# Kernel tuning notes

Hardware: AMD Instinct MI355X
Metric: run time of the kernel (lower is better)

The kernel has to match this reference:

```python
import jax, jax.numpy as jnp
import numpy as np

NUM_HEADS = 12
HEAD_DIM = 64
HIDDEN = 768
SLOT_DIM = 30
BS = 8
FULL = SLOT_DIM * BS  # 240
SLOT_LEN = 32
LEN0 = 512   # slot-broadcast cache length
LEN1 = 128   # per-sample cache length


def tf_slot(x, slot_dim):
    # (slot_dim*bs, H, L, h) -> (bs, H, slot_dim*L, h)
    full, nh, L, h = x.shape
    bs = full // slot_dim
    x = x.reshape(slot_dim, bs, nh, L, h).transpose(1, 2, 0, 3, 4)
    return x.reshape(bs, nh, slot_dim * L, h)


def back_slot(x, slot_dim):
    # (bs, H, slot_dim*L, h) -> (slot_dim*bs, H, L, h)
    bs, nh, total, h = x.shape
    L = total // slot_dim
    x = x.reshape(bs, nh, slot_dim, L, h).transpose(2, 0, 1, 3, 4)
    return x.reshape(slot_dim * bs, nh, L, h)


def setup_inputs() -> dict:
    key = jax.random.key(0)
    ks = jax.random.split(key, 12)
    s = 0.02
    return {
        "hidden_states": jax.random.normal(ks[0], (FULL, SLOT_LEN, HIDDEN), jnp.float32),
        "attention_mask": jnp.zeros((FULL, 1, 1, LEN0 + LEN1 + SLOT_LEN), jnp.float32),
        "cache0_key": jax.random.normal(ks[1], (BS, NUM_HEADS, LEN0, HEAD_DIM), jnp.float32),
        "cache0_value": jax.random.normal(ks[2], (BS, NUM_HEADS, LEN0, HEAD_DIM), jnp.float32),
        "cache1_key": jax.random.normal(ks[3], (FULL, NUM_HEADS, LEN1, HEAD_DIM), jnp.float32),
        "cache1_value": jax.random.normal(ks[4], (FULL, NUM_HEADS, LEN1, HEAD_DIM), jnp.float32),
        "Wq": jax.random.normal(ks[5], (HIDDEN, HIDDEN), jnp.float32) * s,
        "bq": jax.random.normal(ks[6], (HIDDEN,), jnp.float32) * s,
        "Wk": jax.random.normal(ks[7], (HIDDEN, HIDDEN), jnp.float32) * s,
        "bk": jax.random.normal(ks[8], (HIDDEN,), jnp.float32) * s,
        "Wv": jax.random.normal(ks[9], (HIDDEN, HIDDEN), jnp.float32) * s,
        "bv": jax.random.normal(ks[10], (HIDDEN,), jnp.float32) * s,
        "slot_dim": SLOT_DIM,
    }


def reference(hidden_states, attention_mask, cache0_key, cache0_value,
              cache1_key, cache1_value, Wq, bq, Wk, bk, Wv, bv, slot_dim):
    B, L, hid = hidden_states.shape

    def split_heads(x):  # (B, L, hid) -> (B, H, L, h)
        return x.reshape(B, L, NUM_HEADS, HEAD_DIM).transpose(0, 2, 1, 3)

    q = split_heads(hidden_states @ Wq + bq)
    k = split_heads(hidden_states @ Wk + bk)
    v = split_heads(hidden_states @ Wv + bv)

    # self-attention scores (B, H, L, L)
    self_scores = jnp.einsum('bhqd,bhkd->bhqk', q, k)

    # cache0: slot-broadcast path (cache batch = bs, queries batch = slot_dim*bs)
    q_tf = tf_slot(q, slot_dim)  # (bs, H, slot_dim*L, h)
    s0 = back_slot(jnp.einsum('bhqd,bhkd->bhqk', q_tf, cache0_key), slot_dim)  # (B,H,L,LEN0)
    # cache1: direct path (matching batch)
    s1 = jnp.einsum('bhqd,bhkd->bhqk', q, cache1_key)  # (B,H,L,LEN1)

    scores = jnp.concatenate([s0, s1, self_scores], axis=-1)
    scores = scores / jnp.sqrt(jnp.float32(HEAD_DIM)) + attention_mask
    probs = jax.nn.softmax(scores, axis=-1)  # single softmax over all KV sources

    len0 = cache0_key.shape[2]
    len1 = cache1_key.shape[2]
    # self context
    ctx = jnp.einsum('bhqk,bhkd->bhqd', probs[..., -L:], v)
    # cache0 context via slot transform
    p0 = tf_slot(probs[..., :len0], slot_dim)  # (bs, H, slot_dim*L, LEN0)
    ctx = ctx + back_slot(jnp.einsum('bhqk,bhkd->bhqd', p0, cache0_value), slot_dim)
    # cache1 context direct
    ctx = ctx + jnp.einsum('bhqk,bhkd->bhqd', probs[..., len0:len0 + len1], cache1_value)

    # (B, H, L, h) -> (B, L, hid)
    return ctx.transpose(0, 2, 1, 3).reshape(B, L, hid)
```

## Files before the change

### kernel.cpp

```cpp
#include <hip/hip_runtime.h>
#include <math.h>

#define NUM_HEADS 12
#define HEAD_DIM  64
#define HIDDEN    768
#define BS        8
#define FULL      240
#define SLOT_LEN  32
#define LEN0      512
#define LEN1      128
#define KTOT      672
#define M_TOK     (FULL * SLOT_LEN)

typedef float f32x4 __attribute__((ext_vector_type(4)));
typedef short s16x8 __attribute__((ext_vector_type(8)));
typedef short s16x4 __attribute__((ext_vector_type(4)));

__device__ __forceinline__ short f2bf(float x) {
    unsigned u = __float_as_uint(x);
    unsigned r = (u + 0x7fffu + ((u >> 16) & 1u)) >> 16;
    return (short)r;
}

__device__ __forceinline__ void gll16(const short* g, short* l) {
    __builtin_amdgcn_global_load_lds(
        (const __attribute__((address_space(1))) unsigned int*)g,
        (__attribute__((address_space(3))) unsigned int*)l, 16, 0, 0);
}

__global__ __launch_bounds__(256) void cast_hs(const float* __restrict__ in,
                                               short* __restrict__ out, int n4) {
    int i = blockIdx.x * 256 + threadIdx.x;
    if (i < n4) {
        float4 v = ((const float4*)in)[i];
        s16x4 o = {f2bf(v.x), f2bf(v.y), f2bf(v.z), f2bf(v.w)};
        ((s16x4*)out)[i] = o;
    }
}

__global__ __launch_bounds__(256) void trans_v0(const float* __restrict__ v0,
                                                short* __restrict__ v0t) {
    __shared__ float tile[32][65];
    const size_t base = (size_t)blockIdx.x * 2048;
    const int t = threadIdx.x;
#pragma unroll
    for (int i = 0; i < 2; ++i) {
        int f = t + i * 256;
        int kr = f >> 4, d4 = (f & 15) * 4;
        float4 v = *(const float4*)&v0[base + kr * 64 + d4];
        tile[kr][d4 + 0] = v.x; tile[kr][d4 + 1] = v.y;
        tile[kr][d4 + 2] = v.z; tile[kr][d4 + 3] = v.w;
    }
    __syncthreads();
#pragma unroll
    for (int i = 0; i < 2; ++i) {
        int g = t + i * 256;
        int d = g >> 3, kr4 = (g & 7) * 4;
        s16x4 o = {f2bf(tile[kr4 + 0][d]), f2bf(tile[kr4 + 1][d]),
                   f2bf(tile[kr4 + 2][d]), f2bf(tile[kr4 + 3][d])};
        *(s16x4*)&v0t[base + d * 32 + kr4] = o;
    }
}

__global__ __launch_bounds__(256) void cast_w_t(const float* __restrict__ Wq,
                                                const float* __restrict__ Wk,
                                                const float* __restrict__ Wv,
                                                short* __restrict__ WtAll) {
    const float* W = (blockIdx.z == 0) ? Wq : (blockIdx.z == 1) ? Wk : Wv;
    short* Wt = WtAll + (size_t)blockIdx.z * HIDDEN * HIDDEN;
    __shared__ __align__(16) float tile[32][33];
    const int kb0 = blockIdx.y * 32, nb0 = blockIdx.x * 32;
    const int r = threadIdx.x >> 3, c4 = (threadIdx.x & 7) * 4;
    float4 v = *(const float4*)&W[(size_t)(kb0 + r) * HIDDEN + nb0 + c4];
    tile[r][c4 + 0] = v.x; tile[r][c4 + 1] = v.y;
    tile[r][c4 + 2] = v.z; tile[r][c4 + 3] = v.w;
    __syncthreads();
    s16x4 o = {f2bf(tile[c4 + 0][r]), f2bf(tile[c4 + 1][r]),
               f2bf(tile[c4 + 2][r]), f2bf(tile[c4 + 3][r])};
    *(s16x4*)&Wt[(size_t)(nb0 + r) * HIDDEN + kb0 + c4] = o;
}

__global__ __launch_bounds__(256) void qkv_mfma(
    const short* __restrict__ hsb, const short* __restrict__ WtAll,
    const float* __restrict__ bq, const float* __restrict__ bk,
    const float* __restrict__ bv,
    short* __restrict__ qo, short* __restrict__ ko, short* __restrict__ vo)
{
    const int z = blockIdx.z;
    const short* Wt = WtAll + (size_t)z * HIDDEN * HIDDEN;
    const float* bias = (z == 0) ? bq : (z == 1) ? bk : bv;
    short* outp = (z == 0) ? qo : (z == 1) ? ko : vo;

    __shared__ __align__(16) short smem[128 * 128];
    short* As = smem;
    short* Bs = smem + 128 * 64;

    const int t = threadIdx.x;
    const int lane = t & 63, w = t >> 6;
    const int l15 = lane & 15, quad = lane >> 4;
    const int mBase = blockIdx.y * 128, nBase = blockIdx.x * 128;
    const int mw = (w & 1) * 64, nw = (w >> 1) * 64;

    const int srow_in = lane >> 3;
    const int scol8 = (lane & 7) ^ srow_in;

    f32x4 acc[4][4];
    const f32x4 z4 = {0.f, 0.f, 0.f, 0.f};
#pragma unroll
    for (int i = 0; i < 4; ++i)
#pragma unroll
        for (int j = 0; j < 4; ++j) acc[i][j] = z4;

    for (int kb = 0; kb < HIDDEN; kb += 64) {
        __syncthreads();
#pragma unroll
        for (int j = 0; j < 4; ++j) {
            int row = w * 32 + j * 8 + srow_in;
            gll16(&hsb[(size_t)(mBase + row) * HIDDEN + kb + scol8 * 8],
                  &As[(w * 32 + j * 8) * 64]);
            gll16(&Wt[(size_t)(nBase + row) * HIDDEN + kb + scol8 * 8],
                  &Bs[(w * 32 + j * 8) * 64]);
        }
        __syncthreads();
#pragma unroll
        for (int kc = 0; kc < 2; ++kc) {
            s16x8 a[4], b[4];
#pragma unroll
            for (int mt = 0; mt < 4; ++mt) {
                int row = mw + mt * 16 + l15;
                int c8 = (kc * 4 + quad) ^ (row & 7);
                a[mt] = *(const s16x8*)&As[row * 64 + c8 * 8];
            }
#pragma unroll
            for (int nt = 0; nt < 4; ++nt) {
                int row = nw + nt * 16 + l15;
                int c8 = (kc * 4 + quad) ^ (row & 7);
                b[nt] = *(const s16x8*)&Bs[row * 64 + c8 * 8];
            }
#pragma unroll
            for (int mt = 0; mt < 4; ++mt)
#pragma unroll
                for (int nt = 0; nt < 4; ++nt)
                    acc[mt][nt] = __builtin_amdgcn_mfma_f32_16x16x32_bf16(
                        a[mt], b[nt], acc[mt][nt], 0, 0, 0);
        }
    }

    __syncthreads();
#pragma unroll
    for (int nt = 0; nt < 4; ++nt) {
        float bvv = bias[nBase + nw + nt * 16 + l15];
        int col = nw + nt * 16 + l15;
#pragma unroll
        for (int mt = 0; mt < 4; ++mt)
#pragma unroll
            for (int r = 0; r < 4; ++r) {
                int row = mw + mt * 16 + quad * 4 + r;
                smem[row * 128 + col] = f2bf(acc[mt][nt][r] + bvv);
            }
    }
    __syncthreads();
#pragma unroll
    for (int i = 0; i < 8; ++i) {
        int f = t + i * 256;
        int row = f >> 4, c8 = (f & 15) * 8;
        uint4 val = *(const uint4*)&smem[row * 128 + c8];
        int m = mBase + row, n = nBase + c8;
        size_t dst = (((size_t)(m >> 5) * NUM_HEADS + (n >> 6)) * SLOT_LEN + (m & 31)) * 64 + (n & 63);
        *(uint4*)&outp[dst] = val;
    }
}

__global__ __launch_bounds__(256) void attn_mfma(
    const short* __restrict__ qb, const short* __restrict__ kbuf,
    const short* __restrict__ vbuf,
    const short* __restrict__ k0c, const short* __restrict__ v0t,
    const float* __restrict__ c1k, const float* __restrict__ c1v,
    const float* __restrict__ mask, float* __restrict__ out)
{
    __shared__ __align__(16) short Klds[4][32][72];
    __shared__ __align__(16) short Vt[4][64][40];
    __shared__ __align__(16) short Plds[4][32][36];

    const int t = threadIdx.x, lane = t & 63, w = t >> 6;
    const int task = blockIdx.x * 4 + w;
    const int B = task / 12, h = task % 12;
    const int l15 = lane & 15, quad = lane >> 4;

    const short* qp  = qb  + (size_t)(B * NUM_HEADS + h) * SLOT_LEN * 64;
    const short* ksp = kbuf + (size_t)(B * NUM_HEADS + h) * SLOT_LEN * 64;
    const short* vsp = vbuf + (size_t)(B * NUM_HEADS + h) * SLOT_LEN * 64;
    const short* k0p = k0c + (size_t)((B & 7) * NUM_HEADS + h) * LEN0 * 64;
    const short* v0p = v0t + (size_t)((B & 7) * NUM_HEADS + h) * LEN0 * 64;
    const float* k1p = c1k + (size_t)(B * NUM_HEADS + h) * LEN1 * 64;
    const float* v1p = c1v + (size_t)(B * NUM_HEADS + h) * LEN1 * 64;
    const float* mp  = mask + (size_t)B * KTOT;

    short (*K)[72] = Klds[w];
    short (*V)[40] = Vt[w];
    short (*P)[36] = Plds[w];

    const int skey = lane >> 4;
    const int sc4 = (lane & 15) << 2;

    const int kkey = lane >> 3, ku = lane & 7;
    const int vd = lane >> 2, vu = lane & 3;

    s16x8 qf[2][2];
#pragma unroll
    for (int qh = 0; qh < 2; ++qh)
#pragma unroll
        for (int kc = 0; kc < 2; ++kc)
            qf[qh][kc] = *(const s16x8*)&qp[(qh * 16 + l15) * 64 + kc * 32 + quad * 8];

    const f32x4 z4 = {0.f, 0.f, 0.f, 0.f};
    f32x4 o[2][4];
    float lpart[2][4];
#pragma unroll
    for (int qh = 0; qh < 2; ++qh) {
#pragma unroll
        for (int dq = 0; dq < 4; ++dq) o[qh][dq] = z4;
#pragma unroll
        for (int r = 0; r < 4; ++r) lpart[qh][r] = 0.f;
    }

    s16x8 kpre[4], vpre[4];
    float4 kreg[8];
    float mreg0, mreg1;

    auto issue_bf = [&](int c) {
        const short* kcb = k0p + c * 2048;
        const short* vcb = v0p + c * 2048;
#pragma unroll
        for (int i = 0; i < 4; ++i) {
            kpre[i] = *(const s16x8*)&kcb[(i * 64 + lane) * 8];
            vpre[i] = *(const s16x8*)&vcb[(i * 64 + lane) * 8];
        }
    };
    auto issue_k1 = [&](int c) {
        const float* sk = k1p + (c - 16) * 2048;
#pragma unroll
        for (int i = 0; i < 8; ++i)
            kreg[i] = *(const float4*)&sk[(i * 4 + skey) * 64 + sc4];
    };
    auto issue_mask = [&](int c) {
        mreg0 = mp[c * 32 + l15];
        mreg1 = mp[c * 32 + 16 + l15];
    };

    issue_bf(0);
    issue_mask(0);

    for (int c = 0; c < 21; ++c) {
        const float mv0 = mreg0, mv1 = mreg1;
        float4 vv[8];
        bool f32path = (c >= 16 && c < 20);

        if (c < 16) {
#pragma unroll
            for (int i = 0; i < 4; ++i)
                *(s16x8*)&K[i * 8 + kkey][ku * 8] = kpre[i];
#pragma unroll
            for (int i = 0; i < 4; ++i)
                *(s16x8*)&V[i * 16 + vd][vu * 8] = vpre[i];
        } else if (c < 20) {
#pragma unroll
            for (int i = 0; i < 8; ++i) {
                s16x4 kk = {f2bf(kreg[i].x), f2bf(kreg[i].y), f2bf(kreg[i].z), f2bf(kreg[i].w)};
                *(s16x4*)&K[i * 4 + skey][sc4] = kk;
            }
            const float* sv = v1p + (c - 16) * 2048;
#pragma unroll
            for (int i = 0; i < 8; ++i)
                vv[i] = *(const float4*)&sv[(i * 4 + skey) * 64 + sc4];
        } else {
#pragma unroll
            for (int i = 0; i < 8; ++i) {
                int key = i * 4 + skey;
                *(s16x4*)&K[key][sc4] = *(const s16x4*)&ksp[key * 64 + sc4];
            }
            short vtmp[32];
#pragma unroll
            for (int key = 0; key < 32; ++key) vtmp[key] = vsp[key * 64 + lane];
#pragma unroll
            for (int k4 = 0; k4 < 8; ++k4) {
                s16x4 vo4 = {vtmp[k4 * 4 + 0], vtmp[k4 * 4 + 1],
                             vtmp[k4 * 4 + 2], vtmp[k4 * 4 + 3]};
                *(s16x4*)&V[lane][k4 * 4] = vo4;
            }
        }

        if (c + 1 < 16)      issue_bf(c + 1);
        else if (c + 1 < 20) issue_k1(c + 1);
        if (c + 1 < 21)      issue_mask(c + 1);

        f32x4 s[2][2];
#pragma unroll
        for (int qh = 0; qh < 2; ++qh)
#pragma unroll
            for (int kh = 0; kh < 2; ++kh) s[qh][kh] = z4;
#pragma unroll
        for (int kh = 0; kh < 2; ++kh) {
            s16x8 kf0 = *(const s16x8*)&K[kh * 16 + l15][quad * 8];
            s16x8 kf1 = *(const s16x8*)&K[kh * 16 + l15][32 + quad * 8];
#pragma unroll
            for (int qh = 0; qh < 2; ++qh) {
                s[qh][kh] = __builtin_amdgcn_mfma_f32_16x16x32_bf16(qf[qh][0], kf0, s[qh][kh], 0, 0, 0);
                s[qh][kh] = __builtin_amdgcn_mfma_f32_16x16x32_bf16(qf[qh][1], kf1, s[qh][kh], 0, 0, 0);
            }
        }

#pragma unroll
        for (int qh = 0; qh < 2; ++qh)
#pragma unroll
            for (int kh = 0; kh < 2; ++kh) {
                float mv = kh ? mv1 : mv0;
#pragma unroll
                for (int r = 0; r < 4; ++r) {
                    float p = __expf(s[qh][kh][r] * 0.125f + mv);
                    lpart[qh][r] += p;
                    P[qh * 16 + quad * 4 + r][kh * 16 + l15] = f2bf(p);
                }
            }

        if (f32path) {
#pragma unroll
            for (int i = 0; i < 8; ++i) {
                int key = i * 4 + skey;
                V[sc4 + 0][key] = f2bf(vv[i].x);
                V[sc4 + 1][key] = f2bf(vv[i].y);
                V[sc4 + 2][key] = f2bf(vv[i].z);
                V[sc4 + 3][key] = f2bf(vv[i].w);
            }
        }

#pragma unroll
        for (int qh = 0; qh < 2; ++qh) {
            s16x4 plo = *(const s16x4*)&P[qh * 16 + l15][quad * 8];
            s16x4 phi = *(const s16x4*)&P[qh * 16 + l15][quad * 8 + 4];
            s16x8 pf = __builtin_shufflevector(plo, phi, 0, 1, 2, 3, 4, 5, 6, 7);
#pragma unroll
            for (int dq = 0; dq < 4; ++dq) {
                s16x8 vf = *(const s16x8*)&V[dq * 16 + l15][quad * 8];
                o[qh][dq] = __builtin_amdgcn_mfma_f32_16x16x32_bf16(pf, vf, o[qh][dq], 0, 0, 0);
            }
        }
    }

    float linv[2][4];
#pragma unroll
    for (int qh = 0; qh < 2; ++qh)
#pragma unroll
        for (int r = 0; r < 4; ++r) {
            float l = lpart[qh][r];
            l += __shfl_xor(l, 1);
            l += __shfl_xor(l, 2);
            l += __shfl_xor(l, 4);
            l += __shfl_xor(l, 8);
            linv[qh][r] = 1.f / l;
        }

#pragma unroll
    for (int qh = 0; qh < 2; ++qh)
#pragma unroll
        for (int dq = 0; dq < 4; ++dq)
#pragma unroll
            for (int r = 0; r < 4; ++r) {
                int row = qh * 16 + quad * 4 + r;
                out[((size_t)B * SLOT_LEN + row) * HIDDEN + h * 64 + dq * 16 + l15] =
                    o[qh][dq][r] * linv[qh][r];
            }
}

extern "C" void kernel_launch(void* const* d_in, const int* in_sizes, int n_in,
                              void* d_out, int out_size, void* d_ws, size_t ws_size,
                              hipStream_t stream) {
    const float* hs   = (const float*)d_in[0];
    const float* mask = (const float*)d_in[1];
    const float* c0k  = (const float*)d_in[2];
    const float* c0v  = (const float*)d_in[3];
    const float* c1k  = (const float*)d_in[4];
    const float* c1v  = (const float*)d_in[5];
    const float* Wq   = (const float*)d_in[6];
    const float* bq   = (const float*)d_in[7];
    const float* Wk   = (const float*)d_in[8];
    const float* bk   = (const float*)d_in[9];
    const float* Wv   = (const float*)d_in[10];
    const float* bv   = (const float*)d_in[11];
    float* out = (float*)d_out;

    short* hsb = (short*)d_ws;
    short* WtA = hsb + (size_t)M_TOK * HIDDEN;
    short* qb  = WtA + (size_t)3 * HIDDEN * HIDDEN;
    short* kbw = qb + (size_t)M_TOK * HIDDEN;
    short* vbw = kbw + (size_t)M_TOK * HIDDEN;
    short* k0c = (short*)d_ws;
    short* v0t = k0c + (size_t)BS * NUM_HEADS * LEN0 * HEAD_DIM;

    cast_hs<<<(M_TOK * HIDDEN / 4 + 255) / 256, 256, 0, stream>>>(hs, hsb, M_TOK * HIDDEN / 4);
    cast_w_t<<<dim3(24, 24, 3), 256, 0, stream>>>(Wq, Wk, Wv, WtA);
    qkv_mfma<<<dim3(HIDDEN / 128, M_TOK / 128, 3), 256, 0, stream>>>(
        hsb, WtA, bq, bk, bv, qb, kbw, vbw);
    {
        int n4 = BS * NUM_HEADS * LEN0 * HEAD_DIM / 4;
        cast_hs<<<(n4 + 255) / 256, 256, 0, stream>>>(c0k, k0c, n4);
        trans_v0<<<BS * NUM_HEADS * (LEN0 / 32), 256, 0, stream>>>(c0v, v0t);
    }
    attn_mfma<<<720, 256, 0, stream>>>(qb, kbw, vbw, k0c, v0t, c1k, c1v, mask, out);
}
```

Baseline: 362.1 us.

## XOR-swizzle LDS tiles for K, V, P and pre-swizzle cache0 layouts

Replaces the padded LDS arrays for K, V and P with unpadded tiles that use XOR swizzling, which avoids bank conflicts while using less shared memory. The cache0 key cast and value transpose kernels now write their output in the swizzled order, so the attention kernel can copy chunks straight into LDS. Softmax switches to exp2 with the log2e factor folded into the scale and the mask. The next-chunk prefetch issue is also moved into each branch. The risk is that the swizzle index maths must match exactly across the producer kernels and every LDS read and write.

```diff
diff --git a/kernel.cpp b/kernel.cpp
--- a/kernel.cpp
+++ b/kernel.cpp
@@ -38,6 +38,19 @@
     }
 }
 
+__global__ __launch_bounds__(256) void cast_k0(const float* __restrict__ k0,
+                                               short* __restrict__ k0c) {
+    const size_t base = (size_t)blockIdx.x * 2048;
+    const int t = threadIdx.x;
+    const int row = t >> 3, c8 = t & 7;
+    const float* src = &k0[base + row * 64 + c8 * 8];
+    float4 a = *(const float4*)src;
+    float4 b = *(const float4*)(src + 4);
+    s16x8 o = {f2bf(a.x), f2bf(a.y), f2bf(a.z), f2bf(a.w),
+               f2bf(b.x), f2bf(b.y), f2bf(b.z), f2bf(b.w)};
+    *(s16x8*)&k0c[base + row * 64 + (size_t)((c8 ^ (row & 7)) * 8)] = o;
+}
+
 __global__ __launch_bounds__(256) void trans_v0(const float* __restrict__ v0,
                                                 short* __restrict__ v0t) {
     __shared__ float tile[32][65];
@@ -58,7 +71,8 @@
         int d = g >> 3, kr4 = (g & 7) * 4;
         s16x4 o = {f2bf(tile[kr4 + 0][d]), f2bf(tile[kr4 + 1][d]),
                    f2bf(tile[kr4 + 2][d]), f2bf(tile[kr4 + 3][d])};
-        *(s16x4*)&v0t[base + d * 32 + kr4] = o;
+        int grp = (kr4 >> 3) ^ ((d >> 1) & 3);
+        *(s16x4*)&v0t[base + d * 32 + grp * 8 + (kr4 & 7)] = o;
     }
 }
 
@@ -178,9 +192,9 @@
     const float* __restrict__ c1k, const float* __restrict__ c1v,
     const float* __restrict__ mask, float* __restrict__ out)
 {
-    __shared__ __align__(16) short Klds[4][32][72];
-    __shared__ __align__(16) short Vt[4][64][40];
-    __shared__ __align__(16) short Plds[4][32][36];
+    __shared__ __align__(16) short Klds[4][32][64];
+    __shared__ __align__(16) short Vt[4][64][32];
+    __shared__ __align__(16) short Plds[4][32][32];
 
     const int t = threadIdx.x, lane = t & 63, w = t >> 6;
     const int task = blockIdx.x * 4 + w;
@@ -196,15 +210,14 @@
     const float* v1p = c1v + (size_t)(B * NUM_HEADS + h) * LEN1 * 64;
     const float* mp  = mask + (size_t)B * KTOT;
 
-    short (*K)[72] = Klds[w];
-    short (*V)[40] = Vt[w];
-    short (*P)[36] = Plds[w];
+    short (*K)[64] = Klds[w];
+    short (*V)[32] = Vt[w];
+    short (*P)[32] = Plds[w];
+    short* Kf = &K[0][0];
+    short* Vf = &V[0][0];
 
     const int skey = lane >> 4;
     const int sc4 = (lane & 15) << 2;
-
-    const int kkey = lane >> 3, ku = lane & 7;
-    const int vd = lane >> 2, vu = lane & 3;
 
     s16x8 qf[2][2];
 #pragma unroll
@@ -227,6 +240,9 @@
     s16x8 kpre[4], vpre[4];
     float4 kreg[8];
     float mreg0, mreg1;
+
+    const float LOG2E = 1.4426950408889634f;
+    const float SCL   = 0.125f * 1.4426950408889634f;
 
     auto issue_bf = [&](int c) {
         const short* kcb = k0p + c * 2048;
@@ -244,8 +260,8 @@
             kreg[i] = *(const float4*)&sk[(i * 4 + skey) * 64 + sc4];
     };
     auto issue_mask = [&](int c) {
-        mreg0 = mp[c * 32 + l15];
-        mreg1 = mp[c * 32 + 16 + l15];
+        mreg0 = mp[c * 32 + l15] * LOG2E;
+        mreg1 = mp[c * 32 + 16 + l15] * LOG2E;
     };
 
     issue_bf(0);
@@ -259,25 +275,30 @@
         if (c < 16) {
 #pragma unroll
             for (int i = 0; i < 4; ++i)
-                *(s16x8*)&K[i * 8 + kkey][ku * 8] = kpre[i];
+                *(s16x8*)&Kf[(i * 64 + lane) * 8] = kpre[i];
 #pragma unroll
             for (int i = 0; i < 4; ++i)
-                *(s16x8*)&V[i * 16 + vd][vu * 8] = vpre[i];
+                *(s16x8*)&Vf[(i * 64 + lane) * 8] = vpre[i];
+            if (c + 1 < 16) issue_bf(c + 1);
+            if (c == 15) issue_k1(16);
         } else if (c < 20) {
 #pragma unroll
             for (int i = 0; i < 8; ++i) {
                 s16x4 kk = {f2bf(kreg[i].x), f2bf(kreg[i].y), f2bf(kreg[i].z), f2bf(kreg[i].w)};
-                *(s16x4*)&K[i * 4 + skey][sc4] = kk;
+                int row = i * 4 + skey;
+                *(s16x4*)&K[row][((l15 >> 1) ^ (row & 7)) * 8 + (l15 & 1) * 4] = kk;
             }
             const float* sv = v1p + (c - 16) * 2048;
 #pragma unroll
             for (int i = 0; i < 8; ++i)
                 vv[i] = *(const float4*)&sv[(i * 4 + skey) * 64 + sc4];
+            if (c + 1 < 20) issue_k1(c + 1);
         } else {
 #pragma unroll
             for (int i = 0; i < 8; ++i) {
                 int key = i * 4 + skey;
-                *(s16x4*)&K[key][sc4] = *(const s16x4*)&ksp[key * 64 + sc4];
+                *(s16x4*)&K[key][((l15 >> 1) ^ (key & 7)) * 8 + (l15 & 1) * 4] =
+                    *(const s16x4*)&ksp[key * 64 + sc4];
             }
             short vtmp[32];
 #pragma unroll
@@ -286,13 +307,12 @@
             for (int k4 = 0; k4 < 8; ++k4) {
                 s16x4 vo4 = {vtmp[k4 * 4 + 0], vtmp[k4 * 4 + 1],
                              vtmp[k4 * 4 + 2], vtmp[k4 * 4 + 3]};
-                *(s16x4*)&V[lane][k4 * 4] = vo4;
-            }
-        }
-
-        if (c + 1 < 16)      issue_bf(c + 1);
-        else if (c + 1 < 20) issue_k1(c + 1);
-        if (c + 1 < 21)      issue_mask(c + 1);
+                int grp = (k4 >> 1) ^ ((lane >> 1) & 3);
+                *(s16x4*)&V[lane][grp * 8 + (k4 & 1) * 4] = vo4;
+            }
+        }
+
+        if (c + 1 < 21) issue_mask(c + 1);
 
         f32x4 s[2][2];
 #pragma unroll
@@ -301,8 +321,9 @@
             for (int kh = 0; kh < 2; ++kh) s[qh][kh] = z4;
 #pragma unroll
         for (int kh = 0; kh < 2; ++kh) {
-            s16x8 kf0 = *(const s16x8*)&K[kh * 16 + l15][quad * 8];
-            s16x8 kf1 = *(const s16x8*)&K[kh * 16 + l15][32 + quad * 8];
+            int rowk = kh * 16 + l15;
+            s16x8 kf0 = *(const s16x8*)&K[rowk][(quad ^ (rowk & 7)) * 8];
+            s16x8 kf1 = *(const s16x8*)&K[rowk][((4 + quad) ^ (rowk & 7)) * 8];
 #pragma unroll
             for (int qh = 0; qh < 2; ++qh) {
                 s[qh][kh] = __builtin_amdgcn_mfma_f32_16x16x32_bf16(qf[qh][0], kf0, s[qh][kh], 0, 0, 0);
@@ -317,9 +338,11 @@
                 float mv = kh ? mv1 : mv0;
 #pragma unroll
                 for (int r = 0; r < 4; ++r) {
-                    float p = __expf(s[qh][kh][r] * 0.125f + mv);
+                    float p = exp2f(fmaf(s[qh][kh][r], SCL, mv));
                     lpart[qh][r] += p;
-                    P[qh * 16 + quad * 4 + r][kh * 16 + l15] = f2bf(p);
+                    int prow = qh * 16 + quad * 4 + r;
+                    int pswz = ((kh * 2 + (l15 >> 3)) ^ ((prow >> 1) & 3)) * 8 + (l15 & 7);
+                    P[prow][pswz] = f2bf(p);
                 }
             }
 
@@ -327,21 +350,27 @@
 #pragma unroll
             for (int i = 0; i < 8; ++i) {
                 int key = i * 4 + skey;
-                V[sc4 + 0][key] = f2bf(vv[i].x);
-                V[sc4 + 1][key] = f2bf(vv[i].y);
-                V[sc4 + 2][key] = f2bf(vv[i].z);
-                V[sc4 + 3][key] = f2bf(vv[i].w);
+                int kg = key >> 3, ks = key & 7;
+#pragma unroll
+                for (int j = 0; j < 4; ++j) {
+                    int rowv = sc4 + j;
+                    float fv = (j == 0) ? vv[i].x : (j == 1) ? vv[i].y : (j == 2) ? vv[i].z : vv[i].w;
+                    V[rowv][(kg ^ ((rowv >> 1) & 3)) * 8 + ks] = f2bf(fv);
+                }
             }
         }
 
 #pragma unroll
         for (int qh = 0; qh < 2; ++qh) {
-            s16x4 plo = *(const s16x4*)&P[qh * 16 + l15][quad * 8];
-            s16x4 phi = *(const s16x4*)&P[qh * 16 + l15][quad * 8 + 4];
+            int prow2 = qh * 16 + l15;
+            int pg = (quad ^ ((l15 >> 1) & 3)) * 8;
+            s16x4 plo = *(const s16x4*)&P[prow2][pg];
+            s16x4 phi = *(const s16x4*)&P[prow2][pg + 4];
             s16x8 pf = __builtin_shufflevector(plo, phi, 0, 1, 2, 3, 4, 5, 6, 7);
 #pragma unroll
             for (int dq = 0; dq < 4; ++dq) {
-                s16x8 vf = *(const s16x8*)&V[dq * 16 + l15][quad * 8];
+                int vrow = dq * 16 + l15;
+                s16x8 vf = *(const s16x8*)&V[vrow][(quad ^ ((l15 >> 1) & 3)) * 8];
                 o[qh][dq] = __builtin_amdgcn_mfma_f32_16x16x32_bf16(pf, vf, o[qh][dq], 0, 0, 0);
             }
         }
@@ -401,10 +430,7 @@
     cast_w_t<<<dim3(24, 24, 3), 256, 0, stream>>>(Wq, Wk, Wv, WtA);
     qkv_mfma<<<dim3(HIDDEN / 128, M_TOK / 128, 3), 256, 0, stream>>>(
         hsb, WtA, bq, bk, bv, qb, kbw, vbw);
-    {
-        int n4 = BS * NUM_HEADS * LEN0 * HEAD_DIM / 4;
-        cast_hs<<<(n4 + 255) / 256, 256, 0, stream>>>(c0k, k0c, n4);
-        trans_v0<<<BS * NUM_HEADS * (LEN0 / 32), 256, 0, stream>>>(c0v, v0t);
-    }
+    cast_k0<<<BS * NUM_HEADS * (LEN0 / 32), 256, 0, stream>>>(c0k, k0c);
+    trans_v0<<<BS * NUM_HEADS * (LEN0 / 32), 256, 0, stream>>>(c0v, v0t);
     attn_mfma<<<720, 256, 0, stream>>>(qb, kbw, vbw, k0c, v0t, c1k, c1v, mask, out);
 }
```

Result: slower. 407.8 us (+12.6%).
